# Kernel optimization log

Hardware: AMD Instinct MI355X
Metric: run time of the kernel (lower is better)

The kernel has to match this reference:

```python
import jax, jax.numpy as jnp
import numpy as np

N = 50000   # nodes
E = 800000  # edges
G = 128     # graphs in batch


def setup_inputs() -> dict:
    key = jax.random.key(0)
    ks = jax.random.split(key, 16)
    def p(k, shape, s=0.1):
        return (jax.random.normal(k, shape, dtype=jnp.float32) * s)
    return dict(
        x=jax.random.normal(ks[0], (N, 4), dtype=jnp.float32),
        edge_index=jax.random.randint(ks[1], (2, E), 0, N, dtype=jnp.int64),
        edge_attr=jax.random.normal(ks[2], (E, 1), dtype=jnp.float32),
        batch=jnp.sort(jax.random.randint(ks[3], (N,), 0, G, dtype=jnp.int64)),
        # conv1: GATv2Conv(4, 16, heads=8, edge_dim=1)
        Wl1=p(ks[4], (4, 128)), bl1=jnp.zeros((128,), jnp.float32),
        Wr1=p(ks[5], (4, 128)), br1=jnp.zeros((128,), jnp.float32),
        We1=p(ks[6], (1, 128)), att1=p(ks[7], (8, 16)),
        bias1=jnp.zeros((128,), jnp.float32),
        # conv2: GATv2Conv(128, 8, heads=1, edge_dim=1)
        Wl2=p(ks[8], (128, 8)), bl2=jnp.zeros((8,), jnp.float32),
        Wr2=p(ks[9], (128, 8)), br2=jnp.zeros((8,), jnp.float32),
        We2=p(ks[10], (1, 8)), att2=p(ks[11], (1, 8)),
        bias2=jnp.zeros((8,), jnp.float32),
        # layer3: Linear(8, 1)
        W3=p(ks[12], (8, 1)), b3=jnp.zeros((1,), jnp.float32),
    )


def _gatv2(x, src, dst, ea, Wl, bl, Wr, br, We, att, bias, heads, out_ch, n):
    """PyG GATv2Conv: add_self_loops(fill_value='mean'), LeakyReLU(0.2) logits,
    segment softmax over target nodes, aggregate lin_l(x_src), concat heads + bias."""
    ones = jnp.ones((src.shape[0],), x.dtype)
    cnt = jax.ops.segment_sum(ones, dst, num_segments=n)           # [N] in-degree
    loop_ea = jax.ops.segment_sum(ea, dst, num_segments=n) / jnp.maximum(cnt, 1.0)[:, None]
    idx = jnp.arange(n)
    s2 = jnp.concatenate([src, idx])                                # [E2]
    d2 = jnp.concatenate([dst, idx])                                # [E2]
    ea2 = jnp.concatenate([ea, loop_ea], axis=0)                    # [E2, edge_dim]
    H, C = heads, out_ch
    xl = (x @ Wl + bl).reshape(n, H, C)                             # lin_l
    xr = (x @ Wr + br).reshape(n, H, C)                             # lin_r
    ee = (ea2 @ We).reshape(-1, H, C)                               # lin_edge (no bias)
    m = jax.nn.leaky_relu(xl[s2] + xr[d2] + ee, 0.2)                # [E2, H, C]
    logits = jnp.einsum('ehc,hc->eh', m, att)                       # [E2, H]
    mx = jax.lax.stop_gradient(jax.ops.segment_max(logits, d2, num_segments=n))
    a = jnp.exp(logits - mx[d2])
    denom = jax.ops.segment_sum(a, d2, num_segments=n)              # [N, H]
    alpha = a / denom[d2]                                           # segment softmax
    out = jax.ops.segment_sum(alpha[:, :, None] * xl[s2], d2, num_segments=n)
    return out.reshape(n, H * C) + bias


def reference(x, edge_index, edge_attr, batch,
              Wl1, bl1, Wr1, br1, We1, att1, bias1,
              Wl2, bl2, Wr2, br2, We2, att2, bias2,
              W3, b3):
    src, dst = edge_index[0], edge_index[1]
    h = jax.nn.elu(_gatv2(x, src, dst, edge_attr, Wl1, bl1, Wr1, br1, We1, att1, bias1, 8, 16, N))
    # F.dropout(p=0.6) is identity in eval mode
    h = jax.nn.elu(_gatv2(h, src, dst, edge_attr, Wl2, bl2, Wr2, br2, We2, att2, bias2, 1, 8, N))
    cnt = jax.ops.segment_sum(jnp.ones((N,), h.dtype), batch, num_segments=G)
    pooled = jax.ops.segment_sum(h, batch, num_segments=G) / jnp.maximum(cnt, 1.0)[:, None]
    return pooled @ W3 + b3
```

## Files before the change

### kernel.cpp

```cpp
#include <hip/hip_runtime.h>
#include <math.h>

#define LOG2E 1.44269504088896340736f

typedef float f32x2 __attribute__((ext_vector_type(2)));
__device__ __forceinline__ f32x2 pkfma(f32x2 a, f32x2 b, f32x2 c) {
    return __builtin_elementwise_fma(a, b, c);
}
__device__ __forceinline__ f32x2 sp(float s) { f32x2 v = {s, s}; return v; }
__device__ __forceinline__ f32x2 lrelu2(f32x2 m) {
    return __builtin_elementwise_max(m, 0.2f * m);
}
__device__ __forceinline__ float fexp2(float x) {
    float r;
    asm("v_exp_f32 %0, %1" : "=v"(r) : "v"(x));
    return r;
}
__device__ __forceinline__ float elu1(float v) {
    return v > 0.0f ? v : fexp2(v * LOG2E) - 1.0f;
}

#define DPPADD(p, ctrl) \
    p += __int_as_float(__builtin_amdgcn_mov_dpp(__float_as_int(p), ctrl, 0xF, 0xF, true))
#define RED8(p) do { DPPADD(p, 0xB1); DPPADD(p, 0x4E); DPPADD(p, 0x141); } while (0)


__global__ void k_bcnt(const int* __restrict__ dst, int* __restrict__ cntmat,
                       int E, int CE, int NBK) {
    __shared__ int cnt[256];
    int t = threadIdx.x;
    if (t < 256) cnt[t] = 0;
    __syncthreads();
    int c = blockIdx.x;
    int lo = c * CE, hi = min(E, lo + CE);
    int len = hi - lo; if (len < 0) len = 0;
    int len4 = len & ~3;
    for (int o = t * 4; o < len4; o += 4096) {
        int4 d4 = *(const int4*)(dst + lo + o);
        atomicAdd(&cnt[d4.x >> 8], 1);
        atomicAdd(&cnt[d4.y >> 8], 1);
        atomicAdd(&cnt[d4.z >> 8], 1);
        atomicAdd(&cnt[d4.w >> 8], 1);
    }
    for (int o = len4 + t; o < len; o += 1024)
        atomicAdd(&cnt[dst[lo + o] >> 8], 1);
    __syncthreads();
    if (t < NBK) cntmat[t * 256 + c] = cnt[t];
}

__global__ void k_scan1(const int* __restrict__ in, int* __restrict__ out,
                        int* __restrict__ blocksum, int L) {
    __shared__ int sm[256];
    int t = threadIdx.x;
    int i = blockIdx.x * 256 + t;
    int v = (i < L) ? in[i] : 0;
    sm[t] = v;
    __syncthreads();
    #pragma unroll
    for (int off = 1; off < 256; off <<= 1) {
        int add = (t >= off) ? sm[t - off] : 0;
        __syncthreads();
        sm[t] += add;
        __syncthreads();
    }
    if (i < L) out[i] = sm[t] - v;
    if (t == 255) blocksum[blockIdx.x] = sm[255];
}

__global__ void k_scan2(int* __restrict__ blocksum, int nb,
                        const float* __restrict__ Wl2, const float* __restrict__ Wr2,
                        float2* __restrict__ Wtile) {
    __shared__ int sm[256];
    int t = threadIdx.x;
    int v = (t < nb) ? blocksum[t] : 0;
    sm[t] = v;
    __syncthreads();
    #pragma unroll
    for (int off = 1; off < 256; off <<= 1) {
        int add = (t >= off) ? sm[t - off] : 0;
        __syncthreads();
        sm[t] += add;
        __syncthreads();
    }
    if (t < nb) blocksum[t] = sm[t] - v;
    #pragma unroll
    for (int i = 0; i < 4; ++i) {
        int idx = t + i * 256;
        int kk = idx >> 6, l = idx & 63;
        int j = l >> 3, sub = l & 7;
        int k = sub + kk * 8;
        Wtile[idx] = make_float2(Wl2[k * 8 + j], Wr2[k * 8 + j]);
    }
}

__global__ void k_part(const int* __restrict__ src, const int* __restrict__ dst,
                       const float* __restrict__ ea, const int* __restrict__ gofs,
                       const int* __restrict__ blocksum,
                       int2* __restrict__ tmp, int E, int CE, int NBK) {
    __shared__ int cur[256];
    int t = threadIdx.x;
    int c = blockIdx.x;
    if (t < NBK) cur[t] = gofs[t * 256 + c] + blocksum[t];
    __syncthreads();
    int lo = c * CE, hi = min(E, lo + CE);
    int len = hi - lo; if (len < 0) len = 0;
    int len4 = len & ~3;
    for (int o = t * 4; o < len4; o += 4096) {
        int e = lo + o;
        int4 s4 = *(const int4*)(src + e);
        int4 d4 = *(const int4*)(dst + e);
        float4 a4 = *(const float4*)(ea + e);
        int p0 = atomicAdd(&cur[d4.x >> 8], 1);
        int p1 = atomicAdd(&cur[d4.y >> 8], 1);
        int p2 = atomicAdd(&cur[d4.z >> 8], 1);
        int p3 = atomicAdd(&cur[d4.w >> 8], 1);
        tmp[p0] = make_int2(((d4.x & 255) << 24) | (s4.x << 4), __float_as_int(a4.x));
        tmp[p1] = make_int2(((d4.y & 255) << 24) | (s4.y << 4), __float_as_int(a4.y));
        tmp[p2] = make_int2(((d4.z & 255) << 24) | (s4.z << 4), __float_as_int(a4.z));
        tmp[p3] = make_int2(((d4.w & 255) << 24) | (s4.w << 4), __float_as_int(a4.w));
    }
    for (int o = len4 + t; o < len; o += 1024) {
        int e = lo + o;
        int d = dst[e];
        int pos = atomicAdd(&cur[d >> 8], 1);
        tmp[pos] = make_int2(((d & 255) << 24) | (src[e] << 4), __float_as_int(ea[e]));
    }
}

__global__ void k_fsort(const int2* __restrict__ tmp, const int* __restrict__ gofs,
                        const int* __restrict__ blocksum,
                        int2* __restrict__ csr, int* __restrict__ row_ptr,
                        float* __restrict__ loop_ea, int N, int E, int NBK) {
    __shared__ int lcnt[256], lofs[256], lcur[256];
    __shared__ float lea[256];
    int bkt = blockIdx.x;
    int t = threadIdx.x;
    int base = gofs[bkt * 256] + blocksum[bkt];
    int endv = (bkt == NBK - 1) ? E : (gofs[(bkt + 1) * 256] + blocksum[bkt + 1]);
    int cnt = endv - base;
    if (t < 256) { lcnt[t] = 0; lea[t] = 0.0f; }
    __syncthreads();
    for (int i = t; i < cnt; i += 1024) {
        int2 e2 = tmp[base + i];
        unsigned dl = (unsigned)e2.x >> 24;
        atomicAdd(&lcnt[dl], 1);
        atomicAdd(&lea[dl], __int_as_float(e2.y));
    }
    __syncthreads();
    int v = (t < 256) ? lcnt[t] : 0;
    if (t < 256) lofs[t] = v;
    __syncthreads();
    #pragma unroll
    for (int off = 1; off < 256; off <<= 1) {
        int add = (t >= off && t < 256) ? lofs[t - off] : 0;
        __syncthreads();
        if (t < 256) lofs[t] += add;
        __syncthreads();
    }
    if (t < 256) {
        int excl = lofs[t] - v;
        int nlo = bkt << 8;
        if (nlo + t < N) {
            row_ptr[nlo + t] = base + excl;
            loop_ea[nlo + t] = lea[t] / fmaxf((float)v, 1.0f);
        }
        lcur[t] = base + excl;
    }
    __syncthreads();
    for (int i = t; i < cnt; i += 1024) {
        int2 e2 = tmp[base + i];
        int dl = (unsigned)e2.x >> 24;
        int pos = atomicAdd(&lcur[dl], 1);
        csr[pos] = make_int2(e2.x & 0x00FFFFFF, e2.y);
    }
    if (bkt == 0 && t == 0) row_ptr[N] = E;
}


__global__ void k_l1_node(const int2* __restrict__ csr, const int* __restrict__ row_ptr,
                          const float* __restrict__ x, const float* __restrict__ loop_ea,
                          const float* __restrict__ Wl1, const float* __restrict__ bl1,
                          const float* __restrict__ Wr1, const float* __restrict__ br1,
                          const float* __restrict__ We1, const float* __restrict__ att1,
                          const float* __restrict__ bias1, const f32x2* __restrict__ Wtile,
                          const float* __restrict__ bl2, const float* __restrict__ br2,
                          float* __restrict__ xl2, float* __restrict__ xr2, int N) {
    __shared__ float hs[4][128];
    __shared__ f32x2 wlds[1024];
    int t = threadIdx.x;
    #pragma unroll
    for (int i = 0; i < 4; ++i) wlds[t + i * 256] = Wtile[t + i * 256];
    __syncthreads();

    int wid = t >> 6;
    int lane = t & 63;
    int node = blockIdx.x * 4 + wid;
    if (node >= N) return;
    node = __builtin_amdgcn_readfirstlane(node);

    const f32x2* Wl1v = (const f32x2*)Wl1;
    f32x2 wl0 = Wl1v[lane],        wl1v = Wl1v[64 + lane];
    f32x2 wl2v = Wl1v[128 + lane], wl3v = Wl1v[192 + lane];
    f32x2 b2 = ((const f32x2*)bl1)[lane];
    float4 xv = *(const float4*)(x + (size_t)node * 4);
    const f32x2* Wr1v = (const f32x2*)Wr1;
    f32x2 rr = ((const f32x2*)br1)[lane];
    rr = pkfma(sp(xv.x), Wr1v[lane],       rr);
    rr = pkfma(sp(xv.y), Wr1v[64 + lane],  rr);
    rr = pkfma(sp(xv.z), Wr1v[128 + lane], rr);
    rr = pkfma(sp(xv.w), Wr1v[192 + lane], rr);
    f32x2 we2 = ((const f32x2*)We1)[lane];
    f32x2 at2 = ((const f32x2*)att1)[lane] * LOG2E;
    const char* xb = (const char*)x;

    #define VL2(xs) pkfma(sp((xs).w), wl3v, pkfma(sp((xs).z), wl2v, \
                    pkfma(sp((xs).y), wl1v, pkfma(sp((xs).x), wl0, b2))))
    #define LOGIT(xs, ee, vl, aa) \
        f32x2 vl = VL2(xs); \
        float aa; \
        { f32x2 m_ = lrelu2(pkfma(sp(ee), we2, vl + rr)); \
          f32x2 q_ = m_ * at2; \
          float p_ = q_.x + q_.y; RED8(p_); aa = fexp2(p_); }

    int start = row_ptr[node];
    int deg   = row_ptr[node + 1] - start;
    const int2* crow = csr + start;

    float eav = loop_ea[node];
    LOGIT(xv, eav, vls, a);
    float den = a;
    f32x2 acc = sp(a) * vls;
    int k = 0;
    for (; k + 8 <= deg; k += 8) {
        int2 q0 = crow[k],     q1 = crow[k + 1], q2 = crow[k + 2], q3 = crow[k + 3];
        int2 q4 = crow[k + 4], q5 = crow[k + 5], q6 = crow[k + 6], q7 = crow[k + 7];
        float4 y0 = *(const float4*)(xb + (unsigned)q0.x);
        float4 y1 = *(const float4*)(xb + (unsigned)q1.x);
        float4 y2 = *(const float4*)(xb + (unsigned)q2.x);
        float4 y3 = *(const float4*)(xb + (unsigned)q3.x);
        float4 y4 = *(const float4*)(xb + (unsigned)q4.x);
        float4 y5 = *(const float4*)(xb + (unsigned)q5.x);
        float4 y6 = *(const float4*)(xb + (unsigned)q6.x);
        float4 y7 = *(const float4*)(xb + (unsigned)q7.x);
        LOGIT(y0, __int_as_float(q0.y), ul0, b0);
        LOGIT(y1, __int_as_float(q1.y), ul1, b1);
        LOGIT(y2, __int_as_float(q2.y), ul2, bb2);
        LOGIT(y3, __int_as_float(q3.y), ul3, b3);
        LOGIT(y4, __int_as_float(q4.y), ul4, b4);
        LOGIT(y5, __int_as_float(q5.y), ul5, b5);
        LOGIT(y6, __int_as_float(q6.y), ul6, b6);
        LOGIT(y7, __int_as_float(q7.y), ul7, b7);
        den += ((b0 + b1) + (bb2 + b3)) + ((b4 + b5) + (b6 + b7));
        acc = pkfma(sp(b0), ul0, acc);
        acc = pkfma(sp(b1), ul1, acc);
        acc = pkfma(sp(bb2), ul2, acc);
        acc = pkfma(sp(b3), ul3, acc);
        acc = pkfma(sp(b4), ul4, acc);
        acc = pkfma(sp(b5), ul5, acc);
        acc = pkfma(sp(b6), ul6, acc);
        acc = pkfma(sp(b7), ul7, acc);
    }
    for (; k + 4 <= deg; k += 4) {
        int2 pr0 = crow[k],     pr1 = crow[k + 1];
        int2 pr2 = crow[k + 2], pr3 = crow[k + 3];
        float4 x0 = *(const float4*)(xb + (unsigned)pr0.x);
        float4 x1 = *(const float4*)(xb + (unsigned)pr1.x);
        float4 x2 = *(const float4*)(xb + (unsigned)pr2.x);
        float4 x3 = *(const float4*)(xb + (unsigned)pr3.x);
        LOGIT(x0, __int_as_float(pr0.y), vl0, a0);
        LOGIT(x1, __int_as_float(pr1.y), vl1, a1);
        LOGIT(x2, __int_as_float(pr2.y), vl2, a2);
        LOGIT(x3, __int_as_float(pr3.y), vl3, a3);
        den += (a0 + a1) + (a2 + a3);
        acc = pkfma(sp(a0), vl0, acc);
        acc = pkfma(sp(a1), vl1, acc);
        acc = pkfma(sp(a2), vl2, acc);
        acc = pkfma(sp(a3), vl3, acc);
    }
    for (; k < deg; ++k) {
        int2 pr = crow[k];
        float4 xs = *(const float4*)(xb + (unsigned)pr.x);
        LOGIT(xs, __int_as_float(pr.y), vls2, aa);
        den += aa;
        acc = pkfma(sp(aa), vls2, acc);
    }
    #undef VL2
    #undef LOGIT
    f32x2 bia = ((const f32x2*)bias1)[lane];
    f32x2 o = pkfma(acc, sp(1.0f / den), bia);
    float o0 = elu1(o.x);
    float o1 = elu1(o.y);
    *(float2*)&hs[wid][lane * 2] = make_float2(o0, o1);

    int j = lane >> 3, sub = lane & 7;
    f32x2 a2 = {0.0f, 0.0f};
    #pragma unroll
    for (int kk = 0; kk < 16; ++kk) {
        float hk = hs[wid][sub + kk * 8];
        a2 = pkfma(sp(hk), wlds[kk * 64 + lane], a2);
    }
    RED8(a2.x);
    RED8(a2.y);
    if (sub == 0) {
        xl2[(size_t)node * 8 + j] = a2.x + bl2[j];
        xr2[(size_t)node * 8 + j] = a2.y + br2[j];
    }
}


__global__ void k_l2_node(const int2* __restrict__ csr, const int* __restrict__ row_ptr,
                          const float* __restrict__ xl2, const float* __restrict__ xr2,
                          const float* __restrict__ loop_ea,
                          const float* __restrict__ We2, const float* __restrict__ att2,
                          const float* __restrict__ bias2, float* __restrict__ h2, int N) {
    int t = blockIdx.x * blockDim.x + threadIdx.x;
    int node = t >> 3;
    int lane = t & 7;
    if (node >= N) return;
    float4 ra = *(const float4*)(xr2 + (size_t)node * 8);
    float4 rb = *(const float4*)(xr2 + (size_t)node * 8 + 4);
    f32x2 rv0 = {ra.x, ra.y}, rv1 = {ra.z, ra.w}, rv2 = {rb.x, rb.y}, rv3 = {rb.z, rb.w};
    f32x2 we0 = ((const f32x2*)We2)[0], we1 = ((const f32x2*)We2)[1];
    f32x2 we2v = ((const f32x2*)We2)[2], we3 = ((const f32x2*)We2)[3];
    f32x2 at0 = ((const f32x2*)att2)[0] * LOG2E, at1 = ((const f32x2*)att2)[1] * LOG2E;
    f32x2 at2v = ((const f32x2*)att2)[2] * LOG2E, at3 = ((const f32x2*)att2)[3] * LOG2E;
    const char* xlb = (const char*)xl2;
    int start = row_ptr[node], deg = row_ptr[node + 1] - start;
    int total = deg + 1;
    float den = 0.0f;
    f32x2 ac0 = {0,0}, ac1 = {0,0}, ac2 = {0,0}, ac3 = {0,0};
    for (int base = 0; base < total; base += 8) {
        int e = base + lane;
        if (e < total) {
            const float* lp;
            float eav;
            if (e < deg) {
                int2 pr = csr[start + e];
                lp = (const float*)(xlb + 2u * (unsigned)pr.x);
                eav = __int_as_float(pr.y);
            } else {
                lp = xl2 + (size_t)node * 8;
                eav = loop_ea[node];
            }
            float4 la = *(const float4*)lp;
            float4 lb = *(const float4*)(lp + 4);
            f32x2 l0 = {la.x, la.y}, l1 = {la.z, la.w};
            f32x2 l2 = {lb.x, lb.y}, l3 = {lb.z, lb.w};
            f32x2 ev = sp(eav);
            f32x2 q = lrelu2(pkfma(ev, we0, l0 + rv0)) * at0;
            q = pkfma(lrelu2(pkfma(ev, we1, l1 + rv1)), at1, q);
            q = pkfma(lrelu2(pkfma(ev, we2v, l2 + rv2)), at2v, q);
            q = pkfma(lrelu2(pkfma(ev, we3, l3 + rv3)), at3, q);
            float a = fexp2(q.x + q.y);
            den += a;
            f32x2 av = sp(a);
            ac0 = pkfma(av, l0, ac0);
            ac1 = pkfma(av, l1, ac1);
            ac2 = pkfma(av, l2, ac2);
            ac3 = pkfma(av, l3, ac3);
        }
    }
    RED8(den);
    float w0 = ac0.x, w1 = ac0.y, w2 = ac1.x, w3 = ac1.y;
    float w4 = ac2.x, w5 = ac2.y, w6 = ac3.x, w7 = ac3.y;
    RED8(w0); RED8(w1); RED8(w2); RED8(w3);
    RED8(w4); RED8(w5); RED8(w6); RED8(w7);
    if (lane == 0) {
        float inv = 1.0f / den;
        float o[8] = {w0, w1, w2, w3, w4, w5, w6, w7};
        #pragma unroll
        for (int cc = 0; cc < 8; ++cc) {
            float v = fmaf(o[cc], inv, bias2[cc]);
            o[cc] = elu1(v);
        }
        *(float4*)(h2 + (size_t)node * 8)     = make_float4(o[0], o[1], o[2], o[3]);
        *(float4*)(h2 + (size_t)node * 8 + 4) = make_float4(o[4], o[5], o[6], o[7]);
    }
}

__global__ void k_pool(const float* __restrict__ h2, const int* __restrict__ batch,
                       const float* __restrict__ W3, const float* __restrict__ b3,
                       float* __restrict__ out, int N) {
    int g = blockIdx.x;
    int lo = 0, hi = N;
    while (lo < hi) { int mid = (lo + hi) >> 1; if (batch[mid] < g) lo = mid + 1; else hi = mid; }
    int start = lo;
    int lo2 = start, hi2 = N;
    while (lo2 < hi2) { int mid = (lo2 + hi2) >> 1; if (batch[mid] < g + 1) lo2 = mid + 1; else hi2 = mid; }
    int end = lo2;
    int cnt = end - start;
    int t = threadIdx.x;
    int c = t & 7, rg = t >> 3;
    float s = 0.0f;
    for (int i = start + rg; i < end; i += 32) s += h2[(size_t)i * 8 + c];
    __shared__ float sm[256];
    sm[t] = s;
    __syncthreads();
    #pragma unroll
    for (int off = 16; off >= 1; off >>= 1) {
        if (rg < off) sm[t] += sm[t + off * 8];
        __syncthreads();
    }
    if (t == 0) {
        float inv = 1.0f / fmaxf((float)cnt, 1.0f);
        float acc = b3[0];
        #pragma unroll
        for (int cc = 0; cc < 8; ++cc) acc = fmaf(sm[cc] * inv, W3[cc], acc);
        out[g] = acc;
    }
}

extern "C" void kernel_launch(void* const* d_in, const int* in_sizes, int n_in,
                              void* d_out, int out_size, void* d_ws, size_t ws_size,
                              hipStream_t stream) {
    const float* x     = (const float*)d_in[0];
    const int*   ei    = (const int*)d_in[1];
    const float* ea    = (const float*)d_in[2];
    const int*   batch = (const int*)d_in[3];
    const float* Wl1 = (const float*)d_in[4];
    const float* bl1 = (const float*)d_in[5];
    const float* Wr1 = (const float*)d_in[6];
    const float* br1 = (const float*)d_in[7];
    const float* We1 = (const float*)d_in[8];
    const float* att1 = (const float*)d_in[9];
    const float* bias1 = (const float*)d_in[10];
    const float* Wl2 = (const float*)d_in[11];
    const float* bl2 = (const float*)d_in[12];
    const float* Wr2 = (const float*)d_in[13];
    const float* br2 = (const float*)d_in[14];
    const float* We2 = (const float*)d_in[15];
    const float* att2 = (const float*)d_in[16];
    const float* bias2 = (const float*)d_in[17];
    const float* W3 = (const float*)d_in[18];
    const float* b3 = (const float*)d_in[19];

    const int N  = in_sizes[0] / 4;
    const int E  = in_sizes[1] / 2;
    const int G  = out_size;
    const int* src = ei;
    const int* dst = ei + E;

    const int NBK = (N + 255) >> 8;
    const int NCH = 256;
    const int CE  = (((E + NCH - 1) / NCH) + 3) & ~3;
    const int L   = NBK * 256;

    #define ALIGN4(v) (((v) + 3) & ~3)
    int* w = (int*)d_ws;
    int* gofs     = w; w += ALIGN4(L + 1);
    int* blocksum = w; w += 256;
    int* row_ptr  = w; w += ALIGN4(N + 1);
    float* loop_ea = (float*)w; w += ALIGN4(N);
    float* xl2 = (float*)w; w += (size_t)N * 8;
    float* xr2 = (float*)w; w += (size_t)N * 8;
    float* h2  = (float*)w; w += (size_t)N * 8;
    float2* Wtile = (float2*)w; w += 2048;
    int2* tmp = (int2*)w; w += (size_t)E * 2;
    int2* csr = (int2*)w; w += (size_t)E * 2;
    #undef ALIGN4

    k_bcnt<<<NCH, 1024, 0, stream>>>(dst, gofs, E, CE, NBK);
    k_scan1<<<NBK, 256, 0, stream>>>(gofs, gofs, blocksum, L);
    k_scan2<<<1, 256, 0, stream>>>(blocksum, NBK, Wl2, Wr2, Wtile);
    k_part<<<NCH, 1024, 0, stream>>>(src, dst, ea, gofs, blocksum, tmp, E, CE, NBK);
    k_fsort<<<NBK, 1024, 0, stream>>>(tmp, gofs, blocksum, csr, row_ptr, loop_ea, N, E, NBK);

    k_l1_node<<<(N + 3) / 4, 256, 0, stream>>>(csr, row_ptr, x, loop_ea,
                                               Wl1, bl1, Wr1, br1, We1, att1, bias1,
                                               (const f32x2*)Wtile, bl2, br2, xl2, xr2, N);
    k_l2_node<<<((size_t)N * 8 + 255) / 256, 256, 0, stream>>>(csr, row_ptr, xl2, xr2,
                                                               loop_ea, We2, att2, bias2, h2, N);
    k_pool<<<G, 256, 0, stream>>>(h2, batch, W3, b3, (float*)d_out, N);
}
```

Baseline: 100.4 us.

## Compute self-loop edge mean inside node kernels and software-pipeline CSR loads

```diff
diff --git a/kernel.cpp b/kernel.cpp
--- a/kernel.cpp
+++ b/kernel.cpp
@@ -130,21 +130,18 @@
 __global__ void k_fsort(const int2* __restrict__ tmp, const int* __restrict__ gofs,
                         const int* __restrict__ blocksum,
                         int2* __restrict__ csr, int* __restrict__ row_ptr,
-                        float* __restrict__ loop_ea, int N, int E, int NBK) {
+                        int N, int E, int NBK) {
     __shared__ int lcnt[256], lofs[256], lcur[256];
-    __shared__ float lea[256];
     int bkt = blockIdx.x;
     int t = threadIdx.x;
     int base = gofs[bkt * 256] + blocksum[bkt];
     int endv = (bkt == NBK - 1) ? E : (gofs[(bkt + 1) * 256] + blocksum[bkt + 1]);
     int cnt = endv - base;
-    if (t < 256) { lcnt[t] = 0; lea[t] = 0.0f; }
+    if (t < 256) lcnt[t] = 0;
     __syncthreads();
     for (int i = t; i < cnt; i += 1024) {
         int2 e2 = tmp[base + i];
-        unsigned dl = (unsigned)e2.x >> 24;
-        atomicAdd(&lcnt[dl], 1);
-        atomicAdd(&lea[dl], __int_as_float(e2.y));
+        atomicAdd(&lcnt[(unsigned)e2.x >> 24], 1);
     }
     __syncthreads();
     int v = (t < 256) ? lcnt[t] : 0;
@@ -160,10 +157,7 @@
     if (t < 256) {
         int excl = lofs[t] - v;
         int nlo = bkt << 8;
-        if (nlo + t < N) {
-            row_ptr[nlo + t] = base + excl;
-            loop_ea[nlo + t] = lea[t] / fmaxf((float)v, 1.0f);
-        }
+        if (nlo + t < N) row_ptr[nlo + t] = base + excl;
         lcur[t] = base + excl;
     }
     __syncthreads();
@@ -178,7 +172,7 @@
 
 
 __global__ void k_l1_node(const int2* __restrict__ csr, const int* __restrict__ row_ptr,
-                          const float* __restrict__ x, const float* __restrict__ loop_ea,
+                          const float* __restrict__ x,
                           const float* __restrict__ Wl1, const float* __restrict__ bl1,
                           const float* __restrict__ Wr1, const float* __restrict__ br1,
                           const float* __restrict__ We1, const float* __restrict__ att1,
@@ -226,63 +220,99 @@
     int deg   = row_ptr[node + 1] - start;
     const int2* crow = csr + start;
 
-    float eav = loop_ea[node];
-    LOGIT(xv, eav, vls, a);
-    float den = a;
-    f32x2 acc = sp(a) * vls;
+    float den = 0.0f;
+    f32x2 acc = {0.0f, 0.0f};
+    float easum = 0.0f;
     int k = 0;
-    for (; k + 8 <= deg; k += 8) {
-        int2 q0 = crow[k],     q1 = crow[k + 1], q2 = crow[k + 2], q3 = crow[k + 3];
-        int2 q4 = crow[k + 4], q5 = crow[k + 5], q6 = crow[k + 6], q7 = crow[k + 7];
-        float4 y0 = *(const float4*)(xb + (unsigned)q0.x);
-        float4 y1 = *(const float4*)(xb + (unsigned)q1.x);
-        float4 y2 = *(const float4*)(xb + (unsigned)q2.x);
-        float4 y3 = *(const float4*)(xb + (unsigned)q3.x);
-        float4 y4 = *(const float4*)(xb + (unsigned)q4.x);
-        float4 y5 = *(const float4*)(xb + (unsigned)q5.x);
-        float4 y6 = *(const float4*)(xb + (unsigned)q6.x);
-        float4 y7 = *(const float4*)(xb + (unsigned)q7.x);
-        LOGIT(y0, __int_as_float(q0.y), ul0, b0);
-        LOGIT(y1, __int_as_float(q1.y), ul1, b1);
-        LOGIT(y2, __int_as_float(q2.y), ul2, bb2);
-        LOGIT(y3, __int_as_float(q3.y), ul3, b3);
-        LOGIT(y4, __int_as_float(q4.y), ul4, b4);
-        LOGIT(y5, __int_as_float(q5.y), ul5, b5);
-        LOGIT(y6, __int_as_float(q6.y), ul6, b6);
-        LOGIT(y7, __int_as_float(q7.y), ul7, b7);
-        den += ((b0 + b1) + (bb2 + b3)) + ((b4 + b5) + (b6 + b7));
-        acc = pkfma(sp(b0), ul0, acc);
-        acc = pkfma(sp(b1), ul1, acc);
-        acc = pkfma(sp(bb2), ul2, acc);
-        acc = pkfma(sp(b3), ul3, acc);
-        acc = pkfma(sp(b4), ul4, acc);
-        acc = pkfma(sp(b5), ul5, acc);
-        acc = pkfma(sp(b6), ul6, acc);
-        acc = pkfma(sp(b7), ul7, acc);
-    }
-    for (; k + 4 <= deg; k += 4) {
-        int2 pr0 = crow[k],     pr1 = crow[k + 1];
-        int2 pr2 = crow[k + 2], pr3 = crow[k + 3];
-        float4 x0 = *(const float4*)(xb + (unsigned)pr0.x);
-        float4 x1 = *(const float4*)(xb + (unsigned)pr1.x);
-        float4 x2 = *(const float4*)(xb + (unsigned)pr2.x);
-        float4 x3 = *(const float4*)(xb + (unsigned)pr3.x);
-        LOGIT(x0, __int_as_float(pr0.y), vl0, a0);
-        LOGIT(x1, __int_as_float(pr1.y), vl1, a1);
-        LOGIT(x2, __int_as_float(pr2.y), vl2, a2);
-        LOGIT(x3, __int_as_float(pr3.y), vl3, a3);
-        den += (a0 + a1) + (a2 + a3);
-        acc = pkfma(sp(a0), vl0, acc);
-        acc = pkfma(sp(a1), vl1, acc);
-        acc = pkfma(sp(a2), vl2, acc);
-        acc = pkfma(sp(a3), vl3, acc);
+    if (deg >= 8) {
+        int2 q0 = crow[0], q1 = crow[1], q2 = crow[2], q3 = crow[3];
+        int2 q4 = crow[4], q5 = crow[5], q6 = crow[6], q7 = crow[7];
+        for (; k + 16 <= deg; k += 8) {
+            float4 y0 = *(const float4*)(xb + (unsigned)q0.x);
+            float4 y1 = *(const float4*)(xb + (unsigned)q1.x);
+            float4 y2 = *(const float4*)(xb + (unsigned)q2.x);
+            float4 y3 = *(const float4*)(xb + (unsigned)q3.x);
+            float4 y4 = *(const float4*)(xb + (unsigned)q4.x);
+            float4 y5 = *(const float4*)(xb + (unsigned)q5.x);
+            float4 y6 = *(const float4*)(xb + (unsigned)q6.x);
+            float4 y7 = *(const float4*)(xb + (unsigned)q7.x);
+            int2 n0 = crow[k + 8],  n1 = crow[k + 9];
+            int2 n2 = crow[k + 10], n3 = crow[k + 11];
+            int2 n4 = crow[k + 12], n5 = crow[k + 13];
+            int2 n6 = crow[k + 14], n7 = crow[k + 15];
+            float e0 = __int_as_float(q0.y), e1 = __int_as_float(q1.y);
+            float e2 = __int_as_float(q2.y), e3 = __int_as_float(q3.y);
+            float e4 = __int_as_float(q4.y), e5 = __int_as_float(q5.y);
+            float e6 = __int_as_float(q6.y), e7 = __int_as_float(q7.y);
+            easum += ((e0 + e1) + (e2 + e3)) + ((e4 + e5) + (e6 + e7));
+            LOGIT(y0, e0, ul0, b0);
+            LOGIT(y1, e1, ul1, b1);
+            LOGIT(y2, e2, ul2, bb2);
+            LOGIT(y3, e3, ul3, b3);
+            LOGIT(y4, e4, ul4, b4);
+            LOGIT(y5, e5, ul5, b5);
+            LOGIT(y6, e6, ul6, b6);
+            LOGIT(y7, e7, ul7, b7);
+            den += ((b0 + b1) + (bb2 + b3)) + ((b4 + b5) + (b6 + b7));
+            acc = pkfma(sp(b0), ul0, acc);
+            acc = pkfma(sp(b1), ul1, acc);
+            acc = pkfma(sp(bb2), ul2, acc);
+            acc = pkfma(sp(b3), ul3, acc);
+            acc = pkfma(sp(b4), ul4, acc);
+            acc = pkfma(sp(b5), ul5, acc);
+            acc = pkfma(sp(b6), ul6, acc);
+            acc = pkfma(sp(b7), ul7, acc);
+            q0 = n0; q1 = n1; q2 = n2; q3 = n3;
+            q4 = n4; q5 = n5; q6 = n6; q7 = n7;
+        }
+        {
+            float4 y0 = *(const float4*)(xb + (unsigned)q0.x);
+            float4 y1 = *(const float4*)(xb + (unsigned)q1.x);
+            float4 y2 = *(const float4*)(xb + (unsigned)q2.x);
+            float4 y3 = *(const float4*)(xb + (unsigned)q3.x);
+            float4 y4 = *(const float4*)(xb + (unsigned)q4.x);
+            float4 y5 = *(const float4*)(xb + (unsigned)q5.x);
+            float4 y6 = *(const float4*)(xb + (unsigned)q6.x);
+            float4 y7 = *(const float4*)(xb + (unsigned)q7.x);
+            float e0 = __int_as_float(q0.y), e1 = __int_as_float(q1.y);
+            float e2 = __int_as_float(q2.y), e3 = __int_as_float(q3.y);
+            float e4 = __int_as_float(q4.y), e5 = __int_as_float(q5.y);
+            float e6 = __int_as_float(q6.y), e7 = __int_as_float(q7.y);
+            easum += ((e0 + e1) + (e2 + e3)) + ((e4 + e5) + (e6 + e7));
+            LOGIT(y0, e0, ul0, b0);
+            LOGIT(y1, e1, ul1, b1);
+            LOGIT(y2, e2, ul2, bb2);
+            LOGIT(y3, e3, ul3, b3);
+            LOGIT(y4, e4, ul4, b4);
+            LOGIT(y5, e5, ul5, b5);
+            LOGIT(y6, e6, ul6, b6);
+            LOGIT(y7, e7, ul7, b7);
+            den += ((b0 + b1) + (bb2 + b3)) + ((b4 + b5) + (b6 + b7));
+            acc = pkfma(sp(b0), ul0, acc);
+            acc = pkfma(sp(b1), ul1, acc);
+            acc = pkfma(sp(bb2), ul2, acc);
+            acc = pkfma(sp(b3), ul3, acc);
+            acc = pkfma(sp(b4), ul4, acc);
+            acc = pkfma(sp(b5), ul5, acc);
+            acc = pkfma(sp(b6), ul6, acc);
+            acc = pkfma(sp(b7), ul7, acc);
+            k += 8;
+        }
     }
     for (; k < deg; ++k) {
         int2 pr = crow[k];
+        float ee = __int_as_float(pr.y);
         float4 xs = *(const float4*)(xb + (unsigned)pr.x);
-        LOGIT(xs, __int_as_float(pr.y), vls2, aa);
+        easum += ee;
+        LOGIT(xs, ee, vls2, aa);
         den += aa;
         acc = pkfma(sp(aa), vls2, acc);
+    }
+    {
+        float eav = easum / fmaxf((float)deg, 1.0f);
+        LOGIT(xv, eav, vls, a);
+        den += a;
+        acc = pkfma(sp(a), vls, acc);
     }
     #undef VL2
     #undef LOGIT
@@ -310,7 +340,6 @@
 
 __global__ void k_l2_node(const int2* __restrict__ csr, const int* __restrict__ row_ptr,
                           const float* __restrict__ xl2, const float* __restrict__ xr2,
-                          const float* __restrict__ loop_ea,
                           const float* __restrict__ We2, const float* __restrict__ att2,
                           const float* __restrict__ bias2, float* __restrict__ h2, int N) {
     int t = blockIdx.x * blockDim.x + threadIdx.x;
@@ -326,22 +355,15 @@
     f32x2 at2v = ((const f32x2*)att2)[2] * LOG2E, at3 = ((const f32x2*)att2)[3] * LOG2E;
     const char* xlb = (const char*)xl2;
     int start = row_ptr[node], deg = row_ptr[node + 1] - start;
-    int total = deg + 1;
-    float den = 0.0f;
+    float den = 0.0f, easum = 0.0f;
     f32x2 ac0 = {0,0}, ac1 = {0,0}, ac2 = {0,0}, ac3 = {0,0};
-    for (int base = 0; base < total; base += 8) {
+    for (int base = 0; base < deg; base += 8) {
         int e = base + lane;
-        if (e < total) {
-            const float* lp;
-            float eav;
-            if (e < deg) {
-                int2 pr = csr[start + e];
-                lp = (const float*)(xlb + 2u * (unsigned)pr.x);
-                eav = __int_as_float(pr.y);
-            } else {
-                lp = xl2 + (size_t)node * 8;
-                eav = loop_ea[node];
-            }
+        if (e < deg) {
+            int2 pr = csr[start + e];
+            const float* lp = (const float*)(xlb + 2u * (unsigned)pr.x);
+            float eav = __int_as_float(pr.y);
+            easum += eav;
             float4 la = *(const float4*)lp;
             float4 lb = *(const float4*)(lp + 4);
             f32x2 l0 = {la.x, la.y}, l1 = {la.z, la.w};
@@ -361,11 +383,29 @@
         }
     }
     RED8(den);
+    RED8(easum);
     float w0 = ac0.x, w1 = ac0.y, w2 = ac1.x, w3 = ac1.y;
     float w4 = ac2.x, w5 = ac2.y, w6 = ac3.x, w7 = ac3.y;
     RED8(w0); RED8(w1); RED8(w2); RED8(w3);
     RED8(w4); RED8(w5); RED8(w6); RED8(w7);
     if (lane == 0) {
+        float eav = easum / fmaxf((float)deg, 1.0f);
+        const float* lp = xl2 + (size_t)node * 8;
+        float4 la = *(const float4*)lp;
+        float4 lb = *(const float4*)(lp + 4);
+        f32x2 l0 = {la.x, la.y}, l1 = {la.z, la.w};
+        f32x2 l2 = {lb.x, lb.y}, l3 = {lb.z, lb.w};
+        f32x2 ev = sp(eav);
+        f32x2 q = lrelu2(pkfma(ev, we0, l0 + rv0)) * at0;
+        q = pkfma(lrelu2(pkfma(ev, we1, l1 + rv1)), at1, q);
+        q = pkfma(lrelu2(pkfma(ev, we2v, l2 + rv2)), at2v, q);
+        q = pkfma(lrelu2(pkfma(ev, we3, l3 + rv3)), at3, q);
+        float a = fexp2(q.x + q.y);
+        den += a;
+        w0 = fmaf(a, la.x, w0); w1 = fmaf(a, la.y, w1);
+        w2 = fmaf(a, la.z, w2); w3 = fmaf(a, la.w, w3);
+        w4 = fmaf(a, lb.x, w4); w5 = fmaf(a, lb.y, w5);
+        w6 = fmaf(a, lb.z, w6); w7 = fmaf(a, lb.w, w7);
         float inv = 1.0f / den;
         float o[8] = {w0, w1, w2, w3, w4, w5, w6, w7};
         #pragma unroll
@@ -450,7 +490,6 @@
     int* gofs     = w; w += ALIGN4(L + 1);
     int* blocksum = w; w += 256;
     int* row_ptr  = w; w += ALIGN4(N + 1);
-    float* loop_ea = (float*)w; w += ALIGN4(N);
     float* xl2 = (float*)w; w += (size_t)N * 8;
     float* xr2 = (float*)w; w += (size_t)N * 8;
     float* h2  = (float*)w; w += (size_t)N * 8;
@@ -463,12 +502,12 @@
     k_scan1<<<NBK, 256, 0, stream>>>(gofs, gofs, blocksum, L);
     k_scan2<<<1, 256, 0, stream>>>(blocksum, NBK, Wl2, Wr2, Wtile);
     k_part<<<NCH, 1024, 0, stream>>>(src, dst, ea, gofs, blocksum, tmp, E, CE, NBK);
-    k_fsort<<<NBK, 1024, 0, stream>>>(tmp, gofs, blocksum, csr, row_ptr, loop_ea, N, E, NBK);
-
-    k_l1_node<<<(N + 3) / 4, 256, 0, stream>>>(csr, row_ptr, x, loop_ea,
+    k_fsort<<<NBK, 1024, 0, stream>>>(tmp, gofs, blocksum, csr, row_ptr, N, E, NBK);
+
+    k_l1_node<<<(N + 3) / 4, 256, 0, stream>>>(csr, row_ptr, x,
                                                Wl1, bl1, Wr1, br1, We1, att1, bias1,
                                                (const f32x2*)Wtile, bl2, br2, xl2, xr2, N);
     k_l2_node<<<((size_t)N * 8 + 255) / 256, 256, 0, stream>>>(csr, row_ptr, xl2, xr2,
-                                                               loop_ea, We2, att2, bias2, h2, N);
+                                                               We2, att2, bias2, h2, N);
     k_pool<<<G, 256, 0, stream>>>(h2, batch, W3, b3, (float*)d_out, N);
 }
```

Measured after the change: 100.1 us. Within noise of the previous version (-0.3%).
